# Performance work log

Hardware: AMD Instinct MI355X
Metric: run time of the kernel (lower is better)

Reference implementation:

```python
import jax, jax.numpy as jnp
import numpy as np

ROT_DEG = 15.0
TRANS_FRAC = 0.1
B, C, H, W = 64, 3, 384, 384


def setup_inputs() -> dict:
    key = jax.random.key(0)
    k1, k2, k3, k4 = jax.random.split(key, 4)
    x = jax.random.uniform(k1, (B, C, H, W), dtype=jnp.float32)
    # per-sample random affine params, mirroring torch.rand()*2-1 scaling
    angles = (jax.random.uniform(k2, (B,), dtype=jnp.float32) * 2 - 1) * ROT_DEG
    dx = (jax.random.uniform(k3, (B,), dtype=jnp.float32) * 2 - 1) * (TRANS_FRAC * W)
    dy = (jax.random.uniform(k4, (B,), dtype=jnp.float32) * 2 - 1) * (TRANS_FRAC * H)
    return {"x": x, "angles": angles, "dx": dx, "dy": dy}


def _affine_sample_one(img, angle_deg, tx, ty):
    # img: (C,H,W). Rotation about image center + pixel translation,
    # bilinear sampling, zeros fill outside (mode='black').
    c_, h, w = img.shape
    cx = (w - 1) * 0.5
    cy = (h - 1) * 0.5
    yo, xo = jnp.meshgrid(
        jnp.arange(h, dtype=img.dtype) - cy,
        jnp.arange(w, dtype=img.dtype) - cx,
        indexing="ij",
    )  # centered output pixel coords, each (H,W)
    rad = angle_deg * (jnp.pi / 180.0)
    co = jnp.cos(rad)
    si = jnp.sin(rad)
    # inverse affine: output pixel -> input source coord (torchvision convention)
    xs = co * (xo - tx) + si * (yo - ty) + cx
    ys = -si * (xo - tx) + co * (yo - ty) + cy
    x0 = jnp.floor(xs)
    y0 = jnp.floor(ys)
    wx = xs - x0
    wy = ys - y0
    x0i = x0.astype(jnp.int32)
    y0i = y0.astype(jnp.int32)

    def gather(yi, xi):
        valid = (xi >= 0) & (xi < w) & (yi >= 0) & (yi < h)
        xc = jnp.clip(xi, 0, w - 1)
        yc = jnp.clip(yi, 0, h - 1)
        v = img[:, yc, xc]  # (C,H,W)
        return v * valid.astype(img.dtype)

    v00 = gather(y0i, x0i)
    v01 = gather(y0i, x0i + 1)
    v10 = gather(y0i + 1, x0i)
    v11 = gather(y0i + 1, x0i + 1)
    return (
        v00 * (1 - wx) * (1 - wy)
        + v01 * wx * (1 - wy)
        + v10 * (1 - wx) * wy
        + v11 * wx * wy
    )


def reference(x, angles, dx, dy):
    y = jax.vmap(_affine_sample_one)(x, angles, dx, dy)
    return jnp.clip(y, 0.0, 1.0)
```

## Files before the change

### kernel.cpp

```cpp
#include <hip/hip_runtime.h>
#include <hip/hip_bf16.h>
#include <math.h>

#define BB 64
#define CC 3
#define HH 384
#define WW 384
#define HW (HH * WW)

#define TILE_W 64
#define TILE_H 24
#define TX_TILES (WW / TILE_W)
#define TY_TILES (HH / TILE_H)
#define TILES_PER_IMG (TX_TILES * TY_TILES)
#define NBLOCKS (BB * TILES_PER_IMG)

#define LW_STRIDE 71
#define LH_MAX 43
#define LCH (LH_MAX * LW_STRIDE)
#define NSTG 6

__global__ __launch_bounds__(512, 8) void GeometricAugment_kernel(
    const float* __restrict__ x,
    const float* __restrict__ angles,
    const float* __restrict__ dx,
    const float* __restrict__ dy,
    float* __restrict__ out) {

    __shared__ float lds[CC * LCH];

    int bid = blockIdx.x;
    int swz = (bid & 7) * (NBLOCKS / 8) + (bid >> 3);

    int b   = swz / TILES_PER_IMG;
    int t   = swz - b * TILES_PER_IMG;
    int tyb = t / TX_TILES;
    int txb = t - tyb * TX_TILES;

    int tid = threadIdx.x;
    int tx  = tid & 63;
    int tyl = tid >> 6;

    const int X0 = txb * TILE_W;
    const int Y0 = tyb * TILE_H;

    const float cx = (WW - 1) * 0.5f;
    const float cy = (HH - 1) * 0.5f;

    float rad = angles[b] * (float)(M_PI / 180.0);
    float si, co;
    __sincosf(rad, &si, &co);
    float txs = dx[b];
    float tys = dy[b];

    float xo0 = (float)X0 - cx - txs;
    float xo1 = (float)(X0 + TILE_W - 1) - cx - txs;
    float yo0 = (float)Y0 - cy - tys;
    float yo1 = (float)(Y0 + TILE_H - 1) - cy - tys;

    float xsA = co * xo0 + si * yo0 + cx;
    float xsB = co * xo1 + si * yo0 + cx;
    float xsC = co * xo0 + si * yo1 + cx;
    float xsD = co * xo1 + si * yo1 + cx;
    float ysA = -si * xo0 + co * yo0 + cy;
    float ysB = -si * xo1 + co * yo0 + cy;
    float ysC = -si * xo0 + co * yo1 + cy;
    float ysD = -si * xo1 + co * yo1 + cy;

    float xsmin = fminf(fminf(xsA, xsB), fminf(xsC, xsD));
    float xsmax = fmaxf(fmaxf(xsA, xsB), fmaxf(xsC, xsD));
    float ysmin = fminf(fminf(ysA, ysB), fminf(ysC, ysD));
    float ysmax = fmaxf(fmaxf(ysA, ysB), fmaxf(ysC, ysD));

    int ximin = (int)floorf(xsmin) - 1;
    int yimin = (int)floorf(ysmin) - 1;
    int LH = (int)floorf(ysmax) + 2 - yimin + 1;
    LH = min(LH, LH_MAX);

    bool interior = (ximin >= 0) && (yimin >= 0) &&
                    (ximin + LW_STRIDE <= WW) && (yimin + LH <= HH);

    const float* imgb = x + (size_t)b * CC * HW;

    int nelem = LH * LW_STRIDE;

    float s0[NSTG], s1[NSTG], s2[NSTG];
    if (interior) {
        const float* srcb = imgb + yimin * WW + ximin;
        #pragma unroll
        for (int k = 0; k < NSTG; ++k) {
            int i = tid + k * 512;
            if (i < nelem) {
                int y  = i / LW_STRIDE;
                int xL = i - y * LW_STRIDE;
                const float* src = srcb + y * WW + xL;
                s0[k] = src[0];
                s1[k] = src[HW];
                s2[k] = src[2 * HW];
            }
        }
    } else {
        #pragma unroll
        for (int k = 0; k < NSTG; ++k) {
            int i = tid + k * 512;
            if (i < nelem) {
                int y  = i / LW_STRIDE;
                int xL = i - y * LW_STRIDE;
                int gy = min(max(yimin + y, 0), HH - 1);
                int gx = min(max(ximin + xL, 0), WW - 1);
                const float* src = imgb + gy * WW + gx;
                s0[k] = src[0];
                s1[k] = src[HW];
                s2[k] = src[2 * HW];
            }
        }
    }
    #pragma unroll
    for (int k = 0; k < NSTG; ++k) {
        int i = tid + k * 512;
        if (i < nelem) {
            lds[i]           = s0[k];
            lds[LCH + i]     = s1[k];
            lds[2 * LCH + i] = s2[k];
        }
    }
    __syncthreads();

    int x_out = X0 + tx;
    float xo = (float)x_out - cx - txs;
    float yo = (float)(Y0 + tyl) - cy - tys;

    float xs =  co * xo + si * yo + cx;
    float ys = -si * xo + co * yo + cy;
    const float dxs = 8.0f * si;
    const float dys = 8.0f * co;

    float* outb = out + (size_t)b * CC * HW + (size_t)Y0 * WW + x_out;

    if (interior) {
        #pragma unroll
        for (int r = 0; r < TILE_H / 8; ++r) {
            float x0f = floorf(xs);
            float y0f = floorf(ys);
            float wx = xs - x0f;
            float wy = ys - y0f;
            int base = ((int)y0f - yimin) * LW_STRIDE + ((int)x0f - ximin);

            #pragma unroll
            for (int c = 0; c < CC; ++c) {
                const float* l = lds + c * LCH + base;
                float v00 = l[0];
                float v01 = l[1];
                float v10 = l[LW_STRIDE];
                float v11 = l[LW_STRIDE + 1];
                float top = v00 + wx * (v01 - v00);
                float bot = v10 + wx * (v11 - v10);
                float v = top + wy * (bot - top);
                v = fminf(fmaxf(v, 0.0f), 1.0f);
                __builtin_nontemporal_store(v, outb + (size_t)c * HW + (size_t)(tyl + r * 8) * WW);
            }
            xs += dxs;
            ys += dys;
        }
    } else {
        #pragma unroll
        for (int r = 0; r < TILE_H / 8; ++r) {
            float x0f = floorf(xs);
            float y0f = floorf(ys);
            float wx = xs - x0f;
            float wy = ys - y0f;
            int x0 = (int)x0f;
            int y0 = (int)y0f;
            int x1 = x0 + 1;
            int y1 = y0 + 1;

            float vx0 = (x0 >= 0 && x0 < WW) ? 1.0f : 0.0f;
            float vx1 = (x1 >= 0 && x1 < WW) ? 1.0f : 0.0f;
            float vy0 = (y0 >= 0 && y0 < HH) ? 1.0f : 0.0f;
            float vy1 = (y1 >= 0 && y1 < HH) ? 1.0f : 0.0f;

            float w00 = (1.0f - wx) * (1.0f - wy) * vx0 * vy0;
            float w01 = wx * (1.0f - wy) * vx1 * vy0;
            float w10 = (1.0f - wx) * wy * vx0 * vy1;
            float w11 = wx * wy * vx1 * vy1;

            int base = (y0 - yimin) * LW_STRIDE + (x0 - ximin);

            #pragma unroll
            for (int c = 0; c < CC; ++c) {
                const float* l = lds + c * LCH + base;
                float v00 = l[0];
                float v01 = l[1];
                float v10 = l[LW_STRIDE];
                float v11 = l[LW_STRIDE + 1];
                float v = v00 * w00 + v01 * w01 + v10 * w10 + v11 * w11;
                v = fminf(fmaxf(v, 0.0f), 1.0f);
                __builtin_nontemporal_store(v, outb + (size_t)c * HW + (size_t)(tyl + r * 8) * WW);
            }
            xs += dxs;
            ys += dys;
        }
    }
}

extern "C" void kernel_launch(void* const* d_in, const int* in_sizes, int n_in,
                              void* d_out, int out_size, void* d_ws, size_t ws_size,
                              hipStream_t stream) {
    const float* x      = (const float*)d_in[0];
    const float* angles = (const float*)d_in[1];
    const float* dx     = (const float*)d_in[2];
    const float* dy     = (const float*)d_in[3];
    float* out = (float*)d_out;

    GeometricAugment_kernel<<<NBLOCKS, 512, 0, stream>>>(x, angles, dx, dy, out);
}
```

Before: 39.78 us.

## Make blocks persistent across a tile row with register-prefetched next tile

Each block now processes a full row of six horizontal tiles instead of one tile, cutting the grid from 6144 blocks to 1024. While computing the current tile out of LDS, it issues global loads for the next tile's source window into registers, then writes them to LDS after a barrier. This is meant to overlap global load latency with interpolation and stores, and to amortize per-block setup. In exchange there are fewer blocks for latency hiding across CUs, an extra barrier per tile, and higher register pressure.

New measurement: 97.79 us. 2.46x slower.

```diff
diff --git a/kernel.cpp b/kernel.cpp
--- a/kernel.cpp
+++ b/kernel.cpp
@@ -10,10 +10,9 @@
 
 #define TILE_W 64
 #define TILE_H 24
-#define TX_TILES (WW / TILE_W)
+#define TX_TILES 6
 #define TY_TILES (HH / TILE_H)
-#define TILES_PER_IMG (TX_TILES * TY_TILES)
-#define NBLOCKS (BB * TILES_PER_IMG)
+#define NBLOCKS (BB * TY_TILES)
 
 #define LW_STRIDE 71
 #define LH_MAX 43
@@ -32,17 +31,14 @@
     int bid = blockIdx.x;
     int swz = (bid & 7) * (NBLOCKS / 8) + (bid >> 3);
 
-    int b   = swz / TILES_PER_IMG;
-    int t   = swz - b * TILES_PER_IMG;
-    int tyb = t / TX_TILES;
-    int txb = t - tyb * TX_TILES;
+    int b = swz >> 4;
+    int j = swz & 15;
 
     int tid = threadIdx.x;
     int tx  = tid & 63;
     int tyl = tid >> 6;
 
-    const int X0 = txb * TILE_W;
-    const int Y0 = tyb * TILE_H;
+    const int Y0 = j * TILE_H;
 
     const float cx = (WW - 1) * 0.5f;
     const float cy = (HH - 1) * 0.5f;
@@ -53,8 +49,8 @@
     float txs = dx[b];
     float tys = dy[b];
 
-    float xo0 = (float)X0 - cx - txs;
-    float xo1 = (float)(X0 + TILE_W - 1) - cx - txs;
+    float xo0 = 0.0f - cx - txs;
+    float xo1 = (float)(TILE_W - 1) - cx - txs;
     float yo0 = (float)Y0 - cy - tys;
     float yo1 = (float)(Y0 + TILE_H - 1) - cy - tys;
 
@@ -72,134 +68,183 @@
     float ysmin = fminf(fminf(ysA, ysB), fminf(ysC, ysD));
     float ysmax = fmaxf(fmaxf(ysA, ysB), fmaxf(ysC, ysD));
 
-    int ximin = (int)floorf(xsmin) - 1;
-    int yimin = (int)floorf(ysmin) - 1;
-    int LH = (int)floorf(ysmax) + 2 - yimin + 1;
-    LH = min(LH, LH_MAX);
-
-    bool interior = (ximin >= 0) && (yimin >= 0) &&
-                    (ximin + LW_STRIDE <= WW) && (yimin + LH <= HH);
+    const float DXC = 64.0f * co;
+    const float DXS = 64.0f * si;
+
+    float xog = (float)tx - cx - txs;
+    float yog = (float)(Y0 + tyl) - cy - tys;
+    float xsg =  co * xog + si * yog + cx;
+    float ysg = -si * xog + co * yog + cy;
+    const float dxs = 8.0f * si;
+    const float dys = 8.0f * co;
 
     const float* imgb = x + (size_t)b * CC * HW;
-
-    int nelem = LH * LW_STRIDE;
+    float* outbase = out + (size_t)b * CC * HW + (size_t)Y0 * WW + tx;
+
+    int  cxi = (int)floorf(xsmin) - 1;
+    int  cyi = (int)floorf(ysmin) - 1;
+    int  cLH = min((int)floorf(ysmax) + 3 - cyi, LH_MAX);
+    bool cInt = (cxi >= 0) && (cyi >= 0) &&
+                (cxi + LW_STRIDE <= WW) && (cyi + cLH <= HH);
 
     float s0[NSTG], s1[NSTG], s2[NSTG];
-    if (interior) {
-        const float* srcb = imgb + yimin * WW + ximin;
+
+    {
+        int nelem = cLH * LW_STRIDE;
+        if (cInt) {
+            const float* srcb = imgb + cyi * WW + cxi;
+            #pragma unroll
+            for (int k = 0; k < NSTG; ++k) {
+                int i = tid + k * 512;
+                if (i < nelem) {
+                    int y  = i / LW_STRIDE;
+                    int xL = i - y * LW_STRIDE;
+                    const float* src = srcb + y * WW + xL;
+                    s0[k] = src[0]; s1[k] = src[HW]; s2[k] = src[2 * HW];
+                }
+            }
+        } else {
+            #pragma unroll
+            for (int k = 0; k < NSTG; ++k) {
+                int i = tid + k * 512;
+                if (i < nelem) {
+                    int y  = i / LW_STRIDE;
+                    int xL = i - y * LW_STRIDE;
+                    int gy = min(max(cyi + y, 0), HH - 1);
+                    int gx = min(max(cxi + xL, 0), WW - 1);
+                    const float* src = imgb + gy * WW + gx;
+                    s0[k] = src[0]; s1[k] = src[HW]; s2[k] = src[2 * HW];
+                }
+            }
+        }
+    }
+
+    for (int it = 0; it < TX_TILES; ++it) {
+        int nelem = cLH * LW_STRIDE;
         #pragma unroll
         for (int k = 0; k < NSTG; ++k) {
             int i = tid + k * 512;
             if (i < nelem) {
-                int y  = i / LW_STRIDE;
-                int xL = i - y * LW_STRIDE;
-                const float* src = srcb + y * WW + xL;
-                s0[k] = src[0];
-                s1[k] = src[HW];
-                s2[k] = src[2 * HW];
-            }
-        }
-    } else {
-        #pragma unroll
-        for (int k = 0; k < NSTG; ++k) {
-            int i = tid + k * 512;
-            if (i < nelem) {
-                int y  = i / LW_STRIDE;
-                int xL = i - y * LW_STRIDE;
-                int gy = min(max(yimin + y, 0), HH - 1);
-                int gx = min(max(ximin + xL, 0), WW - 1);
-                const float* src = imgb + gy * WW + gx;
-                s0[k] = src[0];
-                s1[k] = src[HW];
-                s2[k] = src[2 * HW];
-            }
-        }
-    }
-    #pragma unroll
-    for (int k = 0; k < NSTG; ++k) {
-        int i = tid + k * 512;
-        if (i < nelem) {
-            lds[i]           = s0[k];
-            lds[LCH + i]     = s1[k];
-            lds[2 * LCH + i] = s2[k];
-        }
-    }
-    __syncthreads();
-
-    int x_out = X0 + tx;
-    float xo = (float)x_out - cx - txs;
-    float yo = (float)(Y0 + tyl) - cy - tys;
-
-    float xs =  co * xo + si * yo + cx;
-    float ys = -si * xo + co * yo + cy;
-    const float dxs = 8.0f * si;
-    const float dys = 8.0f * co;
-
-    float* outb = out + (size_t)b * CC * HW + (size_t)Y0 * WW + x_out;
-
-    if (interior) {
-        #pragma unroll
-        for (int r = 0; r < TILE_H / 8; ++r) {
-            float x0f = floorf(xs);
-            float y0f = floorf(ys);
-            float wx = xs - x0f;
-            float wy = ys - y0f;
-            int base = ((int)y0f - yimin) * LW_STRIDE + ((int)x0f - ximin);
-
-            #pragma unroll
-            for (int c = 0; c < CC; ++c) {
-                const float* l = lds + c * LCH + base;
-                float v00 = l[0];
-                float v01 = l[1];
-                float v10 = l[LW_STRIDE];
-                float v11 = l[LW_STRIDE + 1];
-                float top = v00 + wx * (v01 - v00);
-                float bot = v10 + wx * (v11 - v10);
-                float v = top + wy * (bot - top);
-                v = fminf(fmaxf(v, 0.0f), 1.0f);
-                __builtin_nontemporal_store(v, outb + (size_t)c * HW + (size_t)(tyl + r * 8) * WW);
-            }
-            xs += dxs;
-            ys += dys;
-        }
-    } else {
-        #pragma unroll
-        for (int r = 0; r < TILE_H / 8; ++r) {
-            float x0f = floorf(xs);
-            float y0f = floorf(ys);
-            float wx = xs - x0f;
-            float wy = ys - y0f;
-            int x0 = (int)x0f;
-            int y0 = (int)y0f;
-            int x1 = x0 + 1;
-            int y1 = y0 + 1;
-
-            float vx0 = (x0 >= 0 && x0 < WW) ? 1.0f : 0.0f;
-            float vx1 = (x1 >= 0 && x1 < WW) ? 1.0f : 0.0f;
-            float vy0 = (y0 >= 0 && y0 < HH) ? 1.0f : 0.0f;
-            float vy1 = (y1 >= 0 && y1 < HH) ? 1.0f : 0.0f;
-
-            float w00 = (1.0f - wx) * (1.0f - wy) * vx0 * vy0;
-            float w01 = wx * (1.0f - wy) * vx1 * vy0;
-            float w10 = (1.0f - wx) * wy * vx0 * vy1;
-            float w11 = wx * wy * vx1 * vy1;
-
-            int base = (y0 - yimin) * LW_STRIDE + (x0 - ximin);
-
-            #pragma unroll
-            for (int c = 0; c < CC; ++c) {
-                const float* l = lds + c * LCH + base;
-                float v00 = l[0];
-                float v01 = l[1];
-                float v10 = l[LW_STRIDE];
-                float v11 = l[LW_STRIDE + 1];
-                float v = v00 * w00 + v01 * w01 + v10 * w10 + v11 * w11;
-                v = fminf(fmaxf(v, 0.0f), 1.0f);
-                __builtin_nontemporal_store(v, outb + (size_t)c * HW + (size_t)(tyl + r * 8) * WW);
-            }
-            xs += dxs;
-            ys += dys;
-        }
+                lds[i]           = s0[k];
+                lds[LCH + i]     = s1[k];
+                lds[2 * LCH + i] = s2[k];
+            }
+        }
+        __syncthreads();
+
+        int nxi = 0, nyi = 0, nLH = 0;
+        bool nInt = false;
+        if (it + 1 < TX_TILES) {
+            xsmin += DXC; xsmax += DXC;
+            ysmin -= DXS; ysmax -= DXS;
+            nxi = (int)floorf(xsmin) - 1;
+            nyi = (int)floorf(ysmin) - 1;
+            nLH = min((int)floorf(ysmax) + 3 - nyi, LH_MAX);
+            nInt = (nxi >= 0) && (nyi >= 0) &&
+                   (nxi + LW_STRIDE <= WW) && (nyi + nLH <= HH);
+            int nel2 = nLH * LW_STRIDE;
+            if (nInt) {
+                const float* srcb = imgb + nyi * WW + nxi;
+                #pragma unroll
+                for (int k = 0; k < NSTG; ++k) {
+                    int i = tid + k * 512;
+                    if (i < nel2) {
+                        int y  = i / LW_STRIDE;
+                        int xL = i - y * LW_STRIDE;
+                        const float* src = srcb + y * WW + xL;
+                        s0[k] = src[0]; s1[k] = src[HW]; s2[k] = src[2 * HW];
+                    }
+                }
+            } else {
+                #pragma unroll
+                for (int k = 0; k < NSTG; ++k) {
+                    int i = tid + k * 512;
+                    if (i < nel2) {
+                        int y  = i / LW_STRIDE;
+                        int xL = i - y * LW_STRIDE;
+                        int gy = min(max(nyi + y, 0), HH - 1);
+                        int gx = min(max(nxi + xL, 0), WW - 1);
+                        const float* src = imgb + gy * WW + gx;
+                        s0[k] = src[0]; s1[k] = src[HW]; s2[k] = src[2 * HW];
+                    }
+                }
+            }
+        }
+
+        float xs = xsg, ys = ysg;
+        float* outb = outbase + it * TILE_W;
+
+        if (cInt) {
+            #pragma unroll
+            for (int r = 0; r < TILE_H / 8; ++r) {
+                float x0f = floorf(xs);
+                float y0f = floorf(ys);
+                float wx = xs - x0f;
+                float wy = ys - y0f;
+                int base = ((int)y0f - cyi) * LW_STRIDE + ((int)x0f - cxi);
+
+                #pragma unroll
+                for (int c = 0; c < CC; ++c) {
+                    const float* l = lds + c * LCH + base;
+                    float v00 = l[0];
+                    float v01 = l[1];
+                    float v10 = l[LW_STRIDE];
+                    float v11 = l[LW_STRIDE + 1];
+                    float top = v00 + wx * (v01 - v00);
+                    float bot = v10 + wx * (v11 - v10);
+                    float v = top + wy * (bot - top);
+                    v = fminf(fmaxf(v, 0.0f), 1.0f);
+                    __builtin_nontemporal_store(v, outb + (size_t)c * HW + (size_t)(tyl + r * 8) * WW);
+                }
+                xs += dxs;
+                ys += dys;
+            }
+        } else {
+            #pragma unroll
+            for (int r = 0; r < TILE_H / 8; ++r) {
+                float x0f = floorf(xs);
+                float y0f = floorf(ys);
+                float wx = xs - x0f;
+                float wy = ys - y0f;
+                int x0 = (int)x0f;
+                int y0 = (int)y0f;
+                int x1 = x0 + 1;
+                int y1 = y0 + 1;
+
+                float vx0 = (x0 >= 0 && x0 < WW) ? 1.0f : 0.0f;
+                float vx1 = (x1 >= 0 && x1 < WW) ? 1.0f : 0.0f;
+                float vy0 = (y0 >= 0 && y0 < HH) ? 1.0f : 0.0f;
+                float vy1 = (y1 >= 0 && y1 < HH) ? 1.0f : 0.0f;
+
+                float w00 = (1.0f - wx) * (1.0f - wy) * vx0 * vy0;
+                float w01 = wx * (1.0f - wy) * vx1 * vy0;
+                float w10 = (1.0f - wx) * wy * vx0 * vy1;
+                float w11 = wx * wy * vx1 * vy1;
+
+                int base = (y0 - cyi) * LW_STRIDE + (x0 - cxi);
+
+                #pragma unroll
+                for (int c = 0; c < CC; ++c) {
+                    const float* l = lds + c * LCH + base;
+                    float v00 = l[0];
+                    float v01 = l[1];
+                    float v10 = l[LW_STRIDE];
+                    float v11 = l[LW_STRIDE + 1];
+                    float v = v00 * w00 + v01 * w01 + v10 * w10 + v11 * w11;
+                    v = fminf(fmaxf(v, 0.0f), 1.0f);
+                    __builtin_nontemporal_store(v, outb + (size_t)c * HW + (size_t)(tyl + r * 8) * WW);
+                }
+                xs += dxs;
+                ys += dys;
+            }
+        }
+
+        if (it + 1 == TX_TILES) break;
+        __syncthreads();
+
+        cxi = nxi; cyi = nyi; cLH = nLH; cInt = nInt;
+        xsg += DXC;
+        ysg -= DXS;
     }
 }
 
```
